# Optimization experiments

Hardware: AMD Instinct MI355X
Metric: run time of the kernel (lower is better)

## Reference

```python
import jax, jax.numpy as jnp
import numpy as np

BETA = 1.0  # config.beta
B, G, K, E2 = 1024, 512, 128, 128


def setup_inputs() -> dict:
    key = jax.random.key(0)
    k1, k2, k3, k4, k5 = jax.random.split(key, 5)
    s = 0.05
    return {
        "images": jax.random.normal(k1, (B, G), dtype=jnp.float32),
        "wimg": jax.random.normal(k2, (G, K), dtype=jnp.float32) * s,    # project.weight.T
        "wrec": jax.random.normal(k3, (K, E2), dtype=jnp.float32) * s,   # rec.weight.T
        "wrec2": jax.random.normal(k4, (K + 1, E2), dtype=jnp.float32) * s,  # rec2.weight.T
        "wimg2": jax.random.normal(k5, (G, K, K + 1), dtype=jnp.float32) * s,  # img2.weight.T.reshape(K+1,K,G).T
    }


def _soft_assign(x, codes):
    # x: [B, D], codes: [D, C] -> softmax over C of -beta * mean_D (x - codes)^2
    xh = -jnp.mean((x[:, :, None] - codes[None]) ** 2, axis=1) * BETA  # [B, C]
    return jax.nn.softmax(xh, axis=-1)


def reference(images, wimg, wrec, wrec2, wimg2):
    # ---- encode ----
    xp = _soft_assign(images, wimg)            # [B, K]
    lat = xp @ wrec                            # [B, E2]
    xp = _soft_assign(lat, wrec.T)             # [B, K] (codes are wrec.T: [E2, K])
    idx = jnp.argmax(xp, axis=-1)              # [B] hard component
    xwimg = jnp.transpose(wimg2[:, idx, :], (1, 0, 2))   # [B, G, K+1]
    base = wimg[:, idx].T[:, :, None]                     # [B, G, 1]
    xd = images[:, :, None] - base - xwimg                # [B, G, K+1]
    xh2 = -jnp.mean(xd ** 2, axis=1) * BETA               # [B, K+1]
    xp2 = jax.nn.softmax(xh2, axis=-1)
    lat2 = xp2 @ wrec2                                    # [B, E2]
    # ---- decode (ret='rec', n_step>=1) ----
    xp_d = _soft_assign(lat, wrec.T)           # [B, K]
    xp2_d = _soft_assign(lat2, wrec2.T)        # [B, K+1]
    wimgg = wimg[:, :, None] + wimg2           # [G, K, K+1]
    # tensordot(xp_d[:, :, None]*xp2_d[:, None, :], wimgg.permute(1,2,0), 2)
    xrec = jnp.einsum('bk,bj,gkj->bg', xp_d, xp2_d, wimgg)  # [B, G]
    # ---- loss ----
    loss = jnp.mean((xrec - images) ** 2, axis=-1)  # [B]
    return loss
```

## Files before the change

kernel.cpp:

```cpp
#include <hip/hip_runtime.h>

#define B_   1024
#define G_   512
#define K_   128
#define J_   129
#define E2_  128
#define KK_  16512
#define KKE_ 16640
#define KKP_ 16896
#define SPLITS 16
#define KCHUNK 1056
#define BK_  32
#define KSTEPS 33
#define GS_  8

using short8 = __attribute__((ext_vector_type(8))) short;
using f32x4  = __attribute__((ext_vector_type(4))) float;

__device__ __forceinline__ float bf2f(unsigned short h){
  return __uint_as_float(((unsigned int)h) << 16);
}
__device__ __forceinline__ unsigned short f2bf(float f){
  unsigned int u = __float_as_uint(f);
  u += 0x7fffu + ((u >> 16) & 1u);
  return (unsigned short)(u >> 16);
}

__device__ __forceinline__ float blockSum512(float v, float* red, int t){
  #pragma unroll
  for (int off = 32; off > 0; off >>= 1) v += __shfl_down(v, off);
  __syncthreads();
  if ((t & 63) == 0) red[t >> 6] = v;
  __syncthreads();
  float r = ((red[0] + red[1]) + (red[2] + red[3]))
          + ((red[4] + red[5]) + (red[6] + red[7]));
  __syncthreads();
  return r;
}
__device__ __forceinline__ float blockMax512(float v, float* red, int t){
  #pragma unroll
  for (int off = 32; off > 0; off >>= 1) v = fmaxf(v, __shfl_down(v, off));
  __syncthreads();
  if ((t & 63) == 0) red[t >> 6] = v;
  __syncthreads();
  float r = fmaxf(fmaxf(fmaxf(red[0], red[1]), fmaxf(red[2], red[3])),
                  fmaxf(fmaxf(red[4], red[5]), fmaxf(red[6], red[7])));
  __syncthreads();
  return r;
}
__device__ __forceinline__ int blockArgmax512(float v, int i, float* redf, int* redi, int t){
  #pragma unroll
  for (int off = 32; off > 0; off >>= 1){
    float ov = __shfl_down(v, off);
    int   oi = __shfl_down(i, off);
    if (ov > v || (ov == v && oi < i)){ v = ov; i = oi; }
  }
  __syncthreads();
  if ((t & 63) == 0){ redf[t >> 6] = v; redi[t >> 6] = i; }
  __syncthreads();
  float bv = redf[0]; int bi = redi[0];
  #pragma unroll
  for (int wv = 1; wv < 8; wv++){
    float ov = redf[wv]; int oi = redi[wv];
    if (ov > bv || (ov == bv && oi < bi)){ bv = ov; bi = oi; }
  }
  __syncthreads();
  return bi;
}

__global__ __launch_bounds__(1024) void norms_kernel(
    const float* __restrict__ wimg, const float* __restrict__ wrec,
    const float* __restrict__ wrec2, float* __restrict__ c1norm,
    float* __restrict__ w3norm, float* __restrict__ w6norm,
    float* __restrict__ wrecT, float* __restrict__ wrec2T){
  int t = threadIdx.x;
  if (blockIdx.x == 0){
    __shared__ float red[8][128];
    int k = t & 127, sl = t >> 7;
    float s = 0.f;
    int g0 = sl * (G_/8);
    for (int g = g0; g < g0 + G_/8; g++){
      float v = wimg[g*K_ + k]; s += v*v;
    }
    red[sl][k] = s;
    __syncthreads();
    if (t < 128){
      float r = 0.f;
      #pragma unroll
      for (int i = 0; i < 8; i++) r += red[i][t];
      c1norm[t] = r;
    }
  } else if (blockIdx.x == 1){
    int wave = t >> 6, lane = t & 63;
    for (int k = wave; k < K_; k += 16){
      float v0 = wrec[k*E2_ + lane], v1 = wrec[k*E2_ + 64 + lane];
      float s = v0*v0 + v1*v1;
      #pragma unroll
      for (int off = 32; off > 0; off >>= 1) s += __shfl_down(s, off);
      if (lane == 0) w3norm[k] = s;
    }
  } else if (blockIdx.x == 2){
    int wave = t >> 6, lane = t & 63;
    for (int j = wave; j < J_; j += 16){
      float v0 = wrec2[j*E2_ + lane], v1 = wrec2[j*E2_ + 64 + lane];
      float s = v0*v0 + v1*v1;
      #pragma unroll
      for (int off = 32; off > 0; off >>= 1) s += __shfl_down(s, off);
      if (lane == 0) w6norm[j] = s;
    }
  } else if (blockIdx.x == 3){
    for (int n = t; n < K_*E2_; n += 1024){
      int k = n >> 7, e = n & 127;
      wrecT[e*K_ + k] = wrec[n];
    }
  } else {
    for (int n = t; n < J_*E2_; n += 1024){
      int j = n >> 7, e = n & 127;
      wrec2T[e*J_ + j] = wrec2[n];
    }
  }
}

__global__ __launch_bounds__(128) void tables_part_kernel(
    const float* __restrict__ wimg2, const float* __restrict__ wimg,
    float* __restrict__ sqp, float* __restrict__ crp,
    unsigned short* __restrict__ W2){
  int n  = blockIdx.x * 128 + threadIdx.x;
  int gs = blockIdx.y;
  int k = n / J_;
  float s0=0,s1=0,s2=0,s3=0, c0=0,c1=0,c2=0,c3=0;
  int gbase = gs * (G_/GS_);
  #pragma unroll 2
  for (int g = gbase; g < gbase + G_/GS_; g += 4){
    float w0 = wimg2[(size_t)(g  )*KK_ + n];
    float w1 = wimg2[(size_t)(g+1)*KK_ + n];
    float w2 = wimg2[(size_t)(g+2)*KK_ + n];
    float w3 = wimg2[(size_t)(g+3)*KK_ + n];
    W2[(size_t)(g  )*KKP_ + n] = f2bf(w0);
    W2[(size_t)(g+1)*KKP_ + n] = f2bf(w1);
    W2[(size_t)(g+2)*KKP_ + n] = f2bf(w2);
    W2[(size_t)(g+3)*KKP_ + n] = f2bf(w3);
    s0 += w0*w0; s1 += w1*w1; s2 += w2*w2; s3 += w3*w3;
    c0 += wimg[(g  )*K_ + k]*w0;
    c1 += wimg[(g+1)*K_ + k]*w1;
    c2 += wimg[(g+2)*K_ + k]*w2;
    c3 += wimg[(g+3)*K_ + k]*w3;
  }
  sqp[(size_t)gs*KK_ + n] = (s0+s1)+(s2+s3);
  crp[(size_t)gs*KK_ + n] = (c0+c1)+(c2+c3);
}
__global__ __launch_bounds__(128) void tables_reduce_kernel(
    const float* __restrict__ sqp, const float* __restrict__ crp,
    float* __restrict__ sq2, float* __restrict__ cross){
  int n = blockIdx.x * 128 + threadIdx.x;
  float s = 0.f, c = 0.f;
  #pragma unroll
  for (int gs = 0; gs < GS_; gs++){
    s += sqp[(size_t)gs*KK_ + n];
    c += crp[(size_t)gs*KK_ + n];
  }
  sq2[n] = s; cross[n] = c;
}

__global__ __launch_bounds__(128) void w2tail_kernel(
    const float* __restrict__ wimg, unsigned short* __restrict__ W2){
  int g = blockIdx.x, t = threadIdx.x;
  unsigned short* dst = W2 + (size_t)g * KKP_;
  dst[KK_ + t]        = f2bf(wimg[g*K_ + t]);
  dst[KKE_ + t]       = 0;
  dst[KKE_ + 128 + t] = 0;
}

__global__ __launch_bounds__(512, 8) void encdec_kernel(
    const float* __restrict__ img,  const float* __restrict__ wimg,
    const float* __restrict__ wrec, const float* __restrict__ wrec2,
    const float* __restrict__ wrecT, const float* __restrict__ wrec2T,
    const unsigned short* __restrict__ W2,
    const float* __restrict__ c1norm, const float* __restrict__ w3norm,
    const float* __restrict__ w6norm, const float* __restrict__ sq2,
    const float* __restrict__ cross, unsigned short* __restrict__ Rm){
  __shared__ float simg[G_];
  __shared__ float sp[K_];
  __shared__ float sqv[J_];
  __shared__ float slat[E2_];
  __shared__ float sd1[K_];
  __shared__ float sh4[4][K_];
  __shared__ float xtra[2];
  __shared__ float redf[8];
  __shared__ int   redi[8];

  int t = threadIdx.x;
  int b = blockIdx.x;
  int tt = t & 127, q = t >> 7;

  simg[t] = img[b*G_ + t];
  __syncthreads();
  float a0 = simg[t];
  float imgnorm = blockSum512(a0*a0, redf, t);

  {
    float d0=0,d1v=0,d2=0,d3v=0;
    int g0 = q * 128;
    const float* wcol = wimg + tt;
    for (int g = g0; g < g0 + 128; g += 4){
      d0  += simg[g  ] * wcol[(g  )*K_];
      d1v += simg[g+1] * wcol[(g+1)*K_];
      d2  += simg[g+2] * wcol[(g+2)*K_];
      d3v += simg[g+3] * wcol[(g+3)*K_];
    }
    sh4[q][tt] = (d0+d1v)+(d2+d3v);
  }
  __syncthreads();
  float d1 = (sh4[0][tt] + sh4[1][tt]) + (sh4[2][tt] + sh4[3][tt]);
  if (q == 0) sd1[tt] = d1;
  float xh1 = -(imgnorm - 2.f*d1 + c1norm[tt]) * (1.f/512.f);
  float m1 = blockMax512(xh1, redf, t);
  float ex1 = expf(xh1 - m1);
  float s1 = blockSum512((q == 0) ? ex1 : 0.f, redf, t);
  if (q == 0) sp[tt] = ex1 / s1;
  __syncthreads();

  {
    float l0=0,l1=0;
    int k0 = q * 32;
    for (int k = k0; k < k0 + 32; k += 2){
      l0 += sp[k  ] * wrec[(k  )*E2_ + tt];
      l1 += sp[k+1] * wrec[(k+1)*E2_ + tt];
    }
    sh4[q][tt] = l0 + l1;
  }
  __syncthreads();
  float lat = (sh4[0][tt] + sh4[1][tt]) + (sh4[2][tt] + sh4[3][tt]);
  if (q == 0) slat[tt] = lat;
  float latnorm = blockSum512((q == 0) ? lat*lat : 0.f, redf, t);

  {
    float l0=0,l1=0;
    int e0 = q * 32;
    const float* rT = wrecT + tt;
    for (int e = e0; e < e0 + 32; e += 2){
      l0 += slat[e  ] * rT[(e  )*K_];
      l1 += slat[e+1] * rT[(e+1)*K_];
    }
    sh4[q][tt] = l0 + l1;
  }
  __syncthreads();
  float d3 = (sh4[0][tt] + sh4[1][tt]) + (sh4[2][tt] + sh4[3][tt]);
  float xh3 = -(latnorm - 2.f*d3 + w3norm[tt]) * (1.f/128.f);
  float m3 = blockMax512(xh3, redf, t);
  float ex3 = expf(xh3 - m3);
  float s3 = blockSum512((q == 0) ? ex3 : 0.f, redf, t);
  if (q == 0) sp[tt] = ex3 / s3;
  int idxb = blockArgmax512(xh3, tt, redf, redi, t);
  float dsq = imgnorm - 2.f*sd1[idxb] + c1norm[idxb];

  {
    const unsigned short* Wb = W2 + (size_t)idxb * J_ + tt;
    float s0=0,s1=0,s2=0,s3=0;
    int g0 = q * 128;
    for (int g = g0; g < g0 + 128; g += 4){
      s0 += simg[g  ] * bf2f(Wb[(size_t)(g  )*KKP_]);
      s1 += simg[g+1] * bf2f(Wb[(size_t)(g+1)*KKP_]);
      s2 += simg[g+2] * bf2f(Wb[(size_t)(g+2)*KKP_]);
      s3 += simg[g+3] * bf2f(Wb[(size_t)(g+3)*KKP_]);
    }
    sh4[q][tt] = (s0+s1)+(s2+s3);
  }
  if (t < 64){
    const unsigned short* Wb8 = W2 + (size_t)idxb * J_ + 128;
    float s = 0.f;
    #pragma unroll
    for (int m = 0; m < 8; m++){
      int g = t + 64*m;
      s += simg[g] * bf2f(Wb8[(size_t)g * KKP_]);
    }
    #pragma unroll
    for (int off = 32; off > 0; off >>= 1) s += __shfl_down(s, off);
    if (t == 0) xtra[0] = s;
  }
  __syncthreads();
  float xh2 = -3e38f;
  if (t < J_){
    float di = (t < 128) ? ((sh4[0][t] + sh4[1][t]) + (sh4[2][t] + sh4[3][t])) : xtra[0];
    int nb = idxb*J_ + t;
    xh2 = -(dsq - 2.f*(di - cross[nb]) + sq2[nb]) * (1.f/512.f);
  }
  float m2 = blockMax512(xh2, redf, t);
  float ea = (t < J_) ? expf(xh2 - m2) : 0.f;
  float s2 = blockSum512(ea, redf, t);
  if (t < J_) sqv[t] = ea / s2;
  __syncthreads();

  {
    float l = 0.f;
    int j0 = (q == 0) ? 0 : (q*32 + 1);
    int j1 = q*32 + 33;
    for (int j = j0; j < j1; j++)
      l += sqv[j] * wrec2[j*E2_ + tt];
    sh4[q][tt] = l;
  }
  __syncthreads();
  float lat2 = (sh4[0][tt] + sh4[1][tt]) + (sh4[2][tt] + sh4[3][tt]);
  if (q == 0) slat[tt] = lat2;
  float l2n = blockSum512((q == 0) ? lat2*lat2 : 0.f, redf, t);

  {
    float l0=0,l1=0;
    int e0 = q * 32;
    const float* rT = wrec2T + tt;
    for (int e = e0; e < e0 + 32; e += 2){
      l0 += slat[e  ] * rT[(e  )*J_];
      l1 += slat[e+1] * rT[(e+1)*J_];
    }
    sh4[q][tt] = l0 + l1;
  }
  if (t < 64){
    float s = slat[t]*wrec2T[t*J_ + 128] + slat[t+64]*wrec2T[(t+64)*J_ + 128];
    #pragma unroll
    for (int off = 32; off > 0; off >>= 1) s += __shfl_down(s, off);
    if (t == 0) xtra[1] = s;
  }
  __syncthreads();
  float xh6 = -3e38f;
  if (t < J_){
    float d6 = (t < 128) ? ((sh4[0][t] + sh4[1][t]) + (sh4[2][t] + sh4[3][t])) : xtra[1];
    xh6 = -(l2n - 2.f*d6 + w6norm[t]) * (1.f/128.f);
  }
  float m6 = blockMax512(xh6, redf, t);
  float e6 = (t < J_) ? expf(xh6 - m6) : 0.f;
  float s6 = blockSum512(e6, redf, t);
  if (t < J_) sqv[t] = e6 / s6;
  __syncthreads();

  unsigned short* Rrow = Rm + (size_t)b * KKP_;
  int k = (t >= 387) ? 3 : (t >= 258) ? 2 : (t >= 129) ? 1 : 0;
  int j = t - k*J_;
  for (int kk = t; kk < KKP_; kk += 512){
    float v = 0.f;
    if (kk < KK_)        v = sp[k] * sqv[j];
    else if (kk < KKE_)  v = sp[kk - KK_];
    Rrow[kk] = f2bf(v);
    if (j < 4){ j += 125; k += 3; } else { j -= 4; k += 4; }
  }
}

__global__ __launch_bounds__(256) void gemm_kernel(
    const unsigned short* __restrict__ Rm, const unsigned short* __restrict__ W2,
    float* __restrict__ part){
  __shared__ __align__(16) unsigned int lds[2*128*20];
  unsigned int* lA = lds;
  unsigned int* lB = lds + 128*20;
  int tid = threadIdx.x;
  int l = tid & 63;
  int w = tid >> 6;
  int wr = (w >> 1) * 64, wc = (w & 1) * 64;
  int b0 = blockIdx.y * 128, g0 = blockIdx.x * 128;
  size_t kkbase = (size_t)blockIdx.z * KCHUNK;

  int srow = tid >> 2, scol = tid & 3;
  const unsigned short* pa = Rm + (size_t)(b0 + srow)*KKP_ + kkbase + scol*8;
  const unsigned short* pb = W2 + (size_t)(g0 + srow)*KKP_ + kkbase + scol*8;
  const size_t half = (size_t)64 * KKP_;
  unsigned int woff = srow*20 + scol*4;

  int lrow = l & 15, lko = (l >> 4) << 2;

  f32x4 zero4 = {0.f, 0.f, 0.f, 0.f};
  f32x4 acc[4][4];
  #pragma unroll
  for (int mi = 0; mi < 4; mi++)
    #pragma unroll
    for (int ni = 0; ni < 4; ni++) acc[mi][ni] = zero4;

  for (int s = 0; s < KSTEPS; s++){
    uint4 va0 = *(const uint4*)pa;
    uint4 va1 = *(const uint4*)(pa + half);
    uint4 vb0 = *(const uint4*)pb;
    uint4 vb1 = *(const uint4*)(pb + half);
    pa += BK_; pb += BK_;
    __syncthreads();
    *(uint4*)(lA + woff)          = va0;
    *(uint4*)(lA + woff + 64*20)  = va1;
    *(uint4*)(lB + woff)          = vb0;
    *(uint4*)(lB + woff + 64*20)  = vb1;
    __syncthreads();
    short8 af[4], bfv[4];
    #pragma unroll
    for (int mi = 0; mi < 4; mi++)
      af[mi] = *(const short8*)(lA + (wr + mi*16 + lrow)*20 + lko);
    #pragma unroll
    for (int ni = 0; ni < 4; ni++)
      bfv[ni] = *(const short8*)(lB + (wc + ni*16 + lrow)*20 + lko);
    #pragma unroll
    for (int mi = 0; mi < 4; mi++)
      #pragma unroll
      for (int ni = 0; ni < 4; ni++)
        acc[mi][ni] = __builtin_amdgcn_mfma_f32_16x16x32_bf16(af[mi], bfv[ni], acc[mi][ni], 0, 0, 0);
  }

  float* P = part + ((size_t)blockIdx.z * B_ + b0) * G_ + g0;
  int rh = (l >> 4) << 2, cl = l & 15;
  #pragma unroll
  for (int mi = 0; mi < 4; mi++)
    #pragma unroll
    for (int ni = 0; ni < 4; ni++)
      #pragma unroll
      for (int r = 0; r < 4; r++){
        int row = wr + mi*16 + rh + r;
        int col = wc + ni*16 + cl;
        P[(size_t)row*G_ + col] = acc[mi][ni][r];
      }
}

__global__ __launch_bounds__(128) void loss_kernel(
    const float* __restrict__ img, const float* __restrict__ part,
    float* __restrict__ out){
  __shared__ float redf[2];
  int t = threadIdx.x, b = blockIdx.x;
  float acc = 0.f;
  for (int g = t; g < G_; g += 128){
    float x = 0.f;
    #pragma unroll
    for (int z = 0; z < SPLITS; z++)
      x += part[((size_t)z*B_ + b)*G_ + g];
    float d = x - img[b*G_ + g];
    acc += d*d;
  }
  #pragma unroll
  for (int off = 32; off > 0; off >>= 1) acc += __shfl_down(acc, off);
  __syncthreads();
  if ((t & 63) == 0) redf[t >> 6] = acc;
  __syncthreads();
  if (t == 0) out[b] = (redf[0] + redf[1]) * (1.f/512.f);
}

extern "C" void kernel_launch(void* const* d_in, const int* in_sizes, int n_in,
                              void* d_out, int out_size, void* d_ws, size_t ws_size,
                              hipStream_t stream){
  (void)in_sizes; (void)n_in; (void)out_size; (void)ws_size;
  const float* img   = (const float*)d_in[0];
  const float* wimg  = (const float*)d_in[1];
  const float* wrec  = (const float*)d_in[2];
  const float* wrec2 = (const float*)d_in[3];
  const float* wimg2 = (const float*)d_in[4];
  float* out = (float*)d_out;

  char* ws = (char*)d_ws;
  size_t off = 0;
  auto alloc = [&](size_t bytes) -> void* {
    void* p = ws + off;
    off += (bytes + 255) & ~(size_t)255;
    return p;
  };
  unsigned short* W2   = (unsigned short*)alloc((size_t)G_ * KKP_ * 2);
  unsigned short* Rm   = (unsigned short*)alloc((size_t)B_ * KKP_ * 2);
  float* part   = (float*)alloc((size_t)SPLITS * B_ * G_ * 4);
  float* sqp    = (float*)alloc((size_t)GS_ * KK_ * 4);
  float* crp    = (float*)alloc((size_t)GS_ * KK_ * 4);
  float* sq2    = (float*)alloc((size_t)KK_ * 4);
  float* cross  = (float*)alloc((size_t)KK_ * 4);
  float* c1norm = (float*)alloc(K_ * 4);
  float* w3norm = (float*)alloc(K_ * 4);
  float* w6norm = (float*)alloc(J_ * 4);
  float* wrecT  = (float*)alloc((size_t)K_ * E2_ * 4);
  float* wrec2T = (float*)alloc((size_t)J_ * E2_ * 4);

  norms_kernel<<<dim3(5), dim3(1024), 0, stream>>>(wimg, wrec, wrec2, c1norm, w3norm, w6norm, wrecT, wrec2T);
  tables_part_kernel<<<dim3(129, GS_), dim3(128), 0, stream>>>(wimg2, wimg, sqp, crp, W2);
  tables_reduce_kernel<<<dim3(129), dim3(128), 0, stream>>>(sqp, crp, sq2, cross);
  w2tail_kernel<<<dim3(512), dim3(128), 0, stream>>>(wimg, W2);
  encdec_kernel<<<dim3(1024), dim3(512), 0, stream>>>(img, wimg, wrec, wrec2, wrecT, wrec2T, W2,
      c1norm, w3norm, w6norm, sq2, cross, Rm);
  gemm_kernel<<<dim3(4, 8, SPLITS), dim3(256), 0, stream>>>(Rm, W2, part);
  loss_kernel<<<dim3(1024), dim3(128), 0, stream>>>(img, part, out);
}
```

Before: 126.1 us.

## Pad W2/Rm rows to even stride and vectorize encoder dot-product loads

Changes the bf16 W2 and Rm layouts so each k-row of the (k,j) product is padded from 129 to 130 entries, making per-row element pairs 4-byte aligned. The encoder then reads wimg as float2 and W2 as packed bf16 pairs, with 8 warp-groups each covering 64 g values and reducing through a new shared buffer. The padding column is zeroed in both operands so the GEMM result is unchanged. The aim is fewer, wider loads in the gather-heavy encoder stage, at the cost of an extra reduction stage and more shared memory.

```diff
diff --git a/kernel.cpp b/kernel.cpp
--- a/kernel.cpp
+++ b/kernel.cpp
@@ -1,18 +1,20 @@
 #include <hip/hip_runtime.h>
 
-#define B_   1024
-#define G_   512
-#define K_   128
-#define J_   129
-#define E2_  128
-#define KK_  16512
-#define KKE_ 16640
-#define KKP_ 16896
+#define B_    1024
+#define G_    512
+#define K_    128
+#define J_    129
+#define JP_   130
+#define E2_   128
+#define KK_   16512
+#define KK2_  16640
+#define KKE2_ 16768
+#define KKP_  16896
 #define SPLITS 16
 #define KCHUNK 1056
-#define BK_  32
+#define BK_   32
 #define KSTEPS 33
-#define GS_  8
+#define GS_   8
 
 using short8 = __attribute__((ext_vector_type(8))) short;
 using f32x4  = __attribute__((ext_vector_type(4))) float;
@@ -128,6 +130,7 @@
   int n  = blockIdx.x * 128 + threadIdx.x;
   int gs = blockIdx.y;
   int k = n / J_;
+  int w2i = n + k;
   float s0=0,s1=0,s2=0,s3=0, c0=0,c1=0,c2=0,c3=0;
   int gbase = gs * (G_/GS_);
   #pragma unroll 2
@@ -136,10 +139,10 @@
     float w1 = wimg2[(size_t)(g+1)*KK_ + n];
     float w2 = wimg2[(size_t)(g+2)*KK_ + n];
     float w3 = wimg2[(size_t)(g+3)*KK_ + n];
-    W2[(size_t)(g  )*KKP_ + n] = f2bf(w0);
-    W2[(size_t)(g+1)*KKP_ + n] = f2bf(w1);
-    W2[(size_t)(g+2)*KKP_ + n] = f2bf(w2);
-    W2[(size_t)(g+3)*KKP_ + n] = f2bf(w3);
+    W2[(size_t)(g  )*KKP_ + w2i] = f2bf(w0);
+    W2[(size_t)(g+1)*KKP_ + w2i] = f2bf(w1);
+    W2[(size_t)(g+2)*KKP_ + w2i] = f2bf(w2);
+    W2[(size_t)(g+3)*KKP_ + w2i] = f2bf(w3);
     s0 += w0*w0; s1 += w1*w1; s2 += w2*w2; s3 += w3*w3;
     c0 += wimg[(g  )*K_ + k]*w0;
     c1 += wimg[(g+1)*K_ + k]*w1;
@@ -166,9 +169,9 @@
     const float* __restrict__ wimg, unsigned short* __restrict__ W2){
   int g = blockIdx.x, t = threadIdx.x;
   unsigned short* dst = W2 + (size_t)g * KKP_;
-  dst[KK_ + t]        = f2bf(wimg[g*K_ + t]);
-  dst[KKE_ + t]       = 0;
-  dst[KKE_ + 128 + t] = 0;
+  dst[KK2_ + t]   = f2bf(wimg[g*K_ + t]);
+  dst[KKE2_ + t]  = 0;
+  dst[t*JP_ + 129] = 0;
 }
 
 __global__ __launch_bounds__(512, 8) void encdec_kernel(
@@ -184,6 +187,7 @@
   __shared__ float sqv[J_];
   __shared__ float slat[E2_];
   __shared__ float sd1[K_];
+  __shared__ float sh8[8][132];
   __shared__ float sh4[4][K_];
   __shared__ float xtra[2];
   __shared__ float redf[8];
@@ -192,6 +196,7 @@
   int t = threadIdx.x;
   int b = blockIdx.x;
   int tt = t & 127, q = t >> 7;
+  int l = t & 63,  gs = t >> 6;
 
   simg[t] = img[b*G_ + t];
   __syncthreads();
@@ -199,19 +204,21 @@
   float imgnorm = blockSum512(a0*a0, redf, t);
 
   {
-    float d0=0,d1v=0,d2=0,d3v=0;
-    int g0 = q * 128;
-    const float* wcol = wimg + tt;
-    for (int g = g0; g < g0 + 128; g += 4){
-      d0  += simg[g  ] * wcol[(g  )*K_];
-      d1v += simg[g+1] * wcol[(g+1)*K_];
-      d2  += simg[g+2] * wcol[(g+2)*K_];
-      d3v += simg[g+3] * wcol[(g+3)*K_];
-    }
-    sh4[q][tt] = (d0+d1v)+(d2+d3v);
-  }
-  __syncthreads();
-  float d1 = (sh4[0][tt] + sh4[1][tt]) + (sh4[2][tt] + sh4[3][tt]);
+    float p0=0, p1=0;
+    int g0 = gs * 64;
+    const float* wbase = wimg + 2*l;
+    #pragma unroll 4
+    for (int g = g0; g < g0 + 64; g++){
+      float2 wv = *(const float2*)(wbase + g*K_);
+      float sv = simg[g];
+      p0 += sv*wv.x; p1 += sv*wv.y;
+    }
+    sh8[gs][2*l]   = p0;
+    sh8[gs][2*l+1] = p1;
+  }
+  __syncthreads();
+  float d1 = ((sh8[0][tt] + sh8[1][tt]) + (sh8[2][tt] + sh8[3][tt]))
+           + ((sh8[4][tt] + sh8[5][tt]) + (sh8[6][tt] + sh8[7][tt]));
   if (q == 0) sd1[tt] = d1;
   float xh1 = -(imgnorm - 2.f*d1 + c1norm[tt]) * (1.f/512.f);
   float m1 = blockMax512(xh1, redf, t);
@@ -255,19 +262,21 @@
   float dsq = imgnorm - 2.f*sd1[idxb] + c1norm[idxb];
 
   {
-    const unsigned short* Wb = W2 + (size_t)idxb * J_ + tt;
-    float s0=0,s1=0,s2=0,s3=0;
-    int g0 = q * 128;
-    for (int g = g0; g < g0 + 128; g += 4){
-      s0 += simg[g  ] * bf2f(Wb[(size_t)(g  )*KKP_]);
-      s1 += simg[g+1] * bf2f(Wb[(size_t)(g+1)*KKP_]);
-      s2 += simg[g+2] * bf2f(Wb[(size_t)(g+2)*KKP_]);
-      s3 += simg[g+3] * bf2f(Wb[(size_t)(g+3)*KKP_]);
-    }
-    sh4[q][tt] = (s0+s1)+(s2+s3);
+    const unsigned short* Wb = W2 + (size_t)idxb * JP_ + 2*l;
+    float p0=0, p1=0;
+    int g0 = gs * 64;
+    #pragma unroll 4
+    for (int g = g0; g < g0 + 64; g++){
+      unsigned int wv = *(const unsigned int*)(Wb + (size_t)g*KKP_);
+      float sv = simg[g];
+      p0 += sv * __uint_as_float(wv << 16);
+      p1 += sv * __uint_as_float(wv & 0xffff0000u);
+    }
+    sh8[gs][2*l]   = p0;
+    sh8[gs][2*l+1] = p1;
   }
   if (t < 64){
-    const unsigned short* Wb8 = W2 + (size_t)idxb * J_ + 128;
+    const unsigned short* Wb8 = W2 + (size_t)idxb * JP_ + 128;
     float s = 0.f;
     #pragma unroll
     for (int m = 0; m < 8; m++){
@@ -281,7 +290,10 @@
   __syncthreads();
   float xh2 = -3e38f;
   if (t < J_){
-    float di = (t < 128) ? ((sh4[0][t] + sh4[1][t]) + (sh4[2][t] + sh4[3][t])) : xtra[0];
+    float di = (t < 128)
+      ? (((sh8[0][t] + sh8[1][t]) + (sh8[2][t] + sh8[3][t]))
+       + ((sh8[4][t] + sh8[5][t]) + (sh8[6][t] + sh8[7][t])))
+      : xtra[0];
     int nb = idxb*J_ + t;
     xh2 = -(dsq - 2.f*(di - cross[nb]) + sq2[nb]) * (1.f/512.f);
   }
@@ -292,12 +304,12 @@
   __syncthreads();
 
   {
-    float l = 0.f;
+    float lv = 0.f;
     int j0 = (q == 0) ? 0 : (q*32 + 1);
     int j1 = q*32 + 33;
     for (int j = j0; j < j1; j++)
-      l += sqv[j] * wrec2[j*E2_ + tt];
-    sh4[q][tt] = l;
+      lv += sqv[j] * wrec2[j*E2_ + tt];
+    sh4[q][tt] = lv;
   }
   __syncthreads();
   float lat2 = (sh4[0][tt] + sh4[1][tt]) + (sh4[2][tt] + sh4[3][tt]);
@@ -333,14 +345,16 @@
   __syncthreads();
 
   unsigned short* Rrow = Rm + (size_t)b * KKP_;
-  int k = (t >= 387) ? 3 : (t >= 258) ? 2 : (t >= 129) ? 1 : 0;
-  int j = t - k*J_;
+  int k = t / JP_;
+  int j = t - k*JP_;
   for (int kk = t; kk < KKP_; kk += 512){
     float v = 0.f;
-    if (kk < KK_)        v = sp[k] * sqv[j];
-    else if (kk < KKE_)  v = sp[kk - KK_];
+    if (kk < KK2_){
+      if (j < J_) v = sp[k] * sqv[j];
+    } else if (kk < KKE2_) v = sp[kk - KK2_];
     Rrow[kk] = f2bf(v);
-    if (j < 4){ j += 125; k += 3; } else { j -= 4; k += 4; }
+    j += 122;
+    if (j >= JP_){ j -= JP_; k += 4; } else k += 3;
   }
 }
 
```

New measurement: 129.6 us. 1.03x slower.
